# Kernel tuning notes

Hardware: AMD Instinct MI355X
Metric: run time of the kernel (lower is better)

The kernel has to match this reference:

```python
import jax, jax.numpy as jnp
import numpy as np

SEQ_LEN = 2048
N_FFT = 4096  # nearest power of two >= 2*SEQ_LEN - 1
K = 24
D_IN = 512
D_OUT = 512
K_U = 3


def setup_inputs() -> dict:
    key = jax.random.key(0)
    k1, k2, k3, k4, k5 = jax.random.split(key, 5)
    x = jax.random.normal(k1, (1, SEQ_LEN, D_IN), dtype=jnp.float32)
    phi = jax.random.normal(k2, (SEQ_LEN, K), dtype=jnp.float32)
    M = jax.random.normal(k3, (D_OUT, D_IN, K_U), dtype=jnp.float32) / D_IN
    M_phi_plus = jax.random.normal(k4, (K, D_IN, D_OUT), dtype=jnp.float32) / 10.0
    M_phi_minus = jax.random.normal(k5, (K, D_IN, D_OUT), dtype=jnp.float32) / 10.0
    return {"x": x, "phi": phi, "M": M, "M_phi_plus": M_phi_plus, "M_phi_minus": M_phi_minus}


def _convolve(u, v, n):
    # u: (bsz, seq, d_in); v: (seq, K) spectral filters
    bsz, seq_len, d_in = u.shape
    Kf = v.shape[1]
    # alternating sign (+1, -1, +1, ...) along time, shape (1, seq, 1, 1)
    sgn = jnp.where(jnp.arange(seq_len) % 2 == 1, -1.0, 1.0).reshape(1, seq_len, 1, 1)
    v_f = jnp.fft.rfft(v.astype(jnp.float32).reshape(1, seq_len, Kf, 1, 1), n=n, axis=1)
    u_exp = jnp.broadcast_to(u[:, :, None, :], (bsz, seq_len, Kf, d_in))
    # stack [u, u*sgn] -> (bsz, seq, K, d_in, 2)
    U = jnp.stack([u_exp, u_exp * sgn], axis=-1).astype(jnp.float32)
    U_f = jnp.fft.rfft(U, n=n, axis=1)
    U_conv = jnp.fft.irfft(v_f * U_f, n=n, axis=1)[:, :seq_len]
    U_plus = U_conv[..., 0]
    U_minus = U_conv[..., 1] * sgn  # (b, seq, K, d_in) * (1, seq, 1, 1)
    return U_plus, U_minus


def _ar_preds(M, x):
    # M: (d_out, d_in, k_u); x: (b, l, d_in)
    # ar[t] = sum_{i=0}^{k_u-1} M[:,:,i] @ x[t-i]  (zero before start)
    b, l, _ = x.shape
    out = jnp.zeros((b, l, M.shape[0]), dtype=x.dtype)
    for i in range(M.shape[-1]):
        x_shift = jnp.pad(x, ((0, 0), (i, 0), (0, 0)))[:, :l]
        out = out + jnp.einsum("bli,oi->blo", x_shift, M[:, :, i])
    return out


def reference(x, phi, M, M_phi_plus, M_phi_minus):
    U_plus, U_minus = _convolve(x, phi, N_FFT)
    spectral_plus = jnp.einsum("blkd,kdo->blo", U_plus, M_phi_plus)
    spectral_minus = jnp.einsum("blkd,kdo->blo", U_minus, M_phi_minus)
    output = spectral_plus + spectral_minus  # use_hankel_L=False
    ar = _ar_preds(M, x)
    return output + ar
```

## Files before the change

kernel.cpp:

```cpp
#include <hip/hip_runtime.h>

typedef __bf16 bf16;
typedef bf16 bf16x8 __attribute__((ext_vector_type(8)));
typedef float floatx16 __attribute__((ext_vector_type(16)));

#define AS1 __attribute__((address_space(1)))
#define AS3 __attribute__((address_space(3)))

#define KTOT 26112

__device__ __forceinline__ void stage_tile(const bf16* g, int ld, bf16* lds, int tid) {
#pragma unroll
    for (int it = 0; it < 4; ++it) {
        int q    = it * 256 + tid;
        int row  = q >> 3;
        int col8 = (q & 7) ^ (row & 7);
        __builtin_amdgcn_global_load_lds(
            (const AS1 void*)(g + (size_t)row * ld + col8 * 8),
            (AS3 void*)(lds + q * 8), 16, 0, 0);
    }
}

__device__ __forceinline__ void mfma_block(const bf16* lA, const bf16* lB,
                                           floatx16 acc[2][2], int lane, int wm, int wn) {
    const int lrow = lane & 31;
    const int lk   = lane >> 5;
#pragma unroll
    for (int s = 0; s < 4; ++s) {
        bf16x8 af[2], bfr[2];
        const int c8 = s * 2 + lk;
#pragma unroll
        for (int mi = 0; mi < 2; ++mi) {
            int r = wm * 64 + mi * 32 + lrow;
            af[mi] = *(const bf16x8*)(lA + r * 64 + ((c8 ^ (r & 7)) << 3));
        }
#pragma unroll
        for (int ni = 0; ni < 2; ++ni) {
            int r = wn * 64 + ni * 32 + lrow;
            bfr[ni] = *(const bf16x8*)(lB + r * 64 + ((c8 ^ (r & 7)) << 3));
        }
#pragma unroll
        for (int mi = 0; mi < 2; ++mi)
#pragma unroll
            for (int ni = 0; ni < 2; ++ni)
                acc[mi][ni] = __builtin_amdgcn_mfma_f32_32x32x16_bf16(
                    af[mi], bfr[ni], acc[mi][ni], 0, 0, 0);
    }
}

#define CD_ROW(r, lane) (((r) & 3) + 8 * ((r) >> 2) + 4 * ((lane) >> 5))

__global__ __launch_bounds__(256) void conv_gemm(const bf16* __restrict__ Tb,
                                                 const bf16* __restrict__ xT2,
                                                 bf16* __restrict__ A2) {
    __shared__ bf16 lA[128 * 64], lB[128 * 64];
    const int tid = threadIdx.x;
    const int lane = tid & 63, wave = tid >> 6, wm = wave & 1, wn = wave >> 1;
    const int bid = blockIdx.x;
    const int a    = 7 - (bid / 384);
    const int rem  = bid % 384;
    const int dblk = rem / 48;
    const int kw   = rem % 48;

    floatx16 acc[2][2];
#pragma unroll
    for (int mi = 0; mi < 2; ++mi)
#pragma unroll
        for (int ni = 0; ni < 2; ++ni)
#pragma unroll
            for (int e = 0; e < 16; ++e) acc[mi][ni][e] = 0.f;

    for (int c = 0; c <= a; ++c) {
        const bf16* Ab = Tb + ((size_t)kw * 8 + (a - c)) * 16384;
        const bf16* Bb = xT2 + (size_t)(dblk * 128) * 1024 + c * 128;
#pragma unroll
        for (int kk = 0; kk < 128; kk += 64) {
            stage_tile(Ab + kk, 128, lA, tid);
            stage_tile(Bb + kk, 1024, lB, tid);
            __syncthreads();
            mfma_block(lA, lB, acc, lane, wm, wn);
            __syncthreads();
        }
    }
    const int w = kw & 1, k = kw >> 1;
    const int kv = w ? (24 + k) : k;
    const int p = dblk >> 2, dbase = (dblk & 3) * 128;
    bf16* Ocol = A2 + (size_t)kv * 512 + dbase;
#pragma unroll
    for (int mi = 0; mi < 2; ++mi)
#pragma unroll
        for (int ni = 0; ni < 2; ++ni)
#pragma unroll
            for (int r = 0; r < 16; ++r) {
                int tau = a * 128 + wm * 64 + mi * 32 + CD_ROW(r, lane);
                int t = 2 * tau + p + w;
                if (t < 2048) {
                    int col = wn * 64 + ni * 32 + (lane & 31);
                    Ocol[(size_t)t * KTOT + col] = (bf16)acc[mi][ni][r];
                }
            }
}

__global__ __launch_bounds__(256) void proj_gemm(const bf16* __restrict__ A2,
                                                 const bf16* __restrict__ B2,
                                                 float* __restrict__ P2) {
    __shared__ bf16 lA[2][128 * 64], lB[2][128 * 64];
    const int tid = threadIdx.x;
    const int lane = tid & 63, wave = tid >> 6, wm = wave & 1, wn = wave >> 1;
    const int bm = blockIdx.x, sp = blockIdx.y, bn = blockIdx.z;
    const bf16* Ab = A2 + (size_t)bm * 128 * KTOT + sp * 3264;
    const bf16* Bb = B2 + (size_t)bn * 128 * KTOT + sp * 3264;

    floatx16 acc[2][2];
#pragma unroll
    for (int mi = 0; mi < 2; ++mi)
#pragma unroll
        for (int ni = 0; ni < 2; ++ni)
#pragma unroll
            for (int e = 0; e < 16; ++e) acc[mi][ni][e] = 0.f;

    stage_tile(Ab,      KTOT, lA[0], tid);
    stage_tile(Bb,      KTOT, lB[0], tid);
    stage_tile(Ab + 64, KTOT, lA[1], tid);
    stage_tile(Bb + 64, KTOT, lB[1], tid);

    int cur = 0;
    for (int t = 0; t < 50; ++t) {
        asm volatile("s_waitcnt vmcnt(8)" ::: "memory");
        __builtin_amdgcn_sched_barrier(0);
        __builtin_amdgcn_s_barrier();
        __builtin_amdgcn_sched_barrier(0);
        __builtin_amdgcn_s_setprio(1);
        mfma_block(lA[cur], lB[cur], acc, lane, wm, wn);
        __builtin_amdgcn_s_setprio(0);
        __builtin_amdgcn_sched_barrier(0);
        __builtin_amdgcn_s_barrier();
        __builtin_amdgcn_sched_barrier(0);
        if (t + 2 < 51) {
            stage_tile(Ab + (size_t)(t + 2) * 64, KTOT, lA[cur], tid);
            stage_tile(Bb + (size_t)(t + 2) * 64, KTOT, lB[cur], tid);
        }
        cur ^= 1;
    }
    asm volatile("s_waitcnt vmcnt(0)" ::: "memory");
    __builtin_amdgcn_sched_barrier(0);
    __builtin_amdgcn_s_barrier();
    __builtin_amdgcn_sched_barrier(0);
    mfma_block(lA[cur], lB[cur], acc, lane, wm, wn);

    float* Pt = P2 + (size_t)sp * 1048576;
#pragma unroll
    for (int mi = 0; mi < 2; ++mi)
#pragma unroll
        for (int ni = 0; ni < 2; ++ni)
#pragma unroll
            for (int r = 0; r < 16; ++r) {
                int t = bm * 128 + wm * 64 + mi * 32 + CD_ROW(r, lane);
                int o = bn * 128 + wn * 64 + ni * 32 + (lane & 31);
                Pt[(size_t)t * 512 + o] = acc[mi][ni][r];
            }
}

__global__ void prep_all(const float* __restrict__ x, const float* __restrict__ phi,
                         const float* __restrict__ M, const float* __restrict__ Mp,
                         const float* __restrict__ Mm, bf16* __restrict__ xT2,
                         bf16* __restrict__ A2, bf16* __restrict__ B2,
                         bf16* __restrict__ Tb) {
    __shared__ float smem[2][64 * 65];
    const int b = blockIdx.x, tid = threadIdx.x;
    if (b < 256) {
        int dpt = (b >> 4) * 64, st = (b & 15) * 64;
        int p = dpt >> 9, dbase = dpt & 511;
#pragma unroll
        for (int it = 0; it < 16; ++it) {
            int q = it * 256 + tid;
            int r = q >> 6, cc = q & 63;
            smem[0][r * 65 + cc] = x[(size_t)(2 * (st + r) + p) * 512 + dbase + cc];
        }
        __syncthreads();
#pragma unroll
        for (int it = 0; it < 2; ++it) {
            int q = it * 256 + tid;
            int r = q >> 3, c8 = q & 7;
            bf16x8 v;
#pragma unroll
            for (int jj = 0; jj < 8; ++jj)
                v[jj] = (bf16)smem[0][(c8 * 8 + jj) * 65 + r];
            *(bf16x8*)&xT2[(size_t)(dpt + r) * 1024 + st + c8 * 8] = v;
        }
    } else if (b < 1792) {
        int idx8 = (b - 256) * 256 + tid;
        int t = idx8 / 192, q = idx8 % 192;
        int i = q >> 6, d8 = (q & 63) * 8;
        bf16x8 v;
        if (t - i >= 0) {
            const float* xp = x + (size_t)(t - i) * 512 + d8;
            float4 f0 = *(const float4*)(xp);
            float4 f1 = *(const float4*)(xp + 4);
            v[0] = (bf16)f0.x; v[1] = (bf16)f0.y; v[2] = (bf16)f0.z; v[3] = (bf16)f0.w;
            v[4] = (bf16)f1.x; v[5] = (bf16)f1.y; v[6] = (bf16)f1.z; v[7] = (bf16)f1.w;
        } else {
#pragma unroll
            for (int jj = 0; jj < 8; ++jj) v[jj] = (bf16)0.f;
        }
        *(bf16x8*)(A2 + (size_t)t * KTOT + 24576 + i * 512 + d8) = v;
    } else if (b < 3328) {
        int b2 = b - 1792;
        int k = b2 >> 6, rem2 = b2 & 63;
        int dt = (rem2 >> 3) * 64, ot = (rem2 & 7) * 64;
        const float* Sp = Mp + (size_t)k * 262144;
        const float* Sm = Mm + (size_t)k * 262144;
#pragma unroll
        for (int it = 0; it < 16; ++it) {
            int q = it * 256 + tid;
            int r = q >> 6, cc = q & 63;
            smem[0][r * 65 + cc] = Sp[(size_t)(dt + r) * 512 + ot + cc];
            smem[1][r * 65 + cc] = Sm[(size_t)(dt + r) * 512 + ot + cc];
        }
        __syncthreads();
#pragma unroll
        for (int it = 0; it < 2; ++it) {
            int q = it * 256 + tid;
            int r = q >> 3, c8 = q & 7;
            bf16x8 vs, vd;
#pragma unroll
            for (int jj = 0; jj < 8; ++jj) {
                float av = smem[0][(c8 * 8 + jj) * 65 + r];
                float bv = smem[1][(c8 * 8 + jj) * 65 + r];
                vs[jj] = (bf16)(av + bv);
                vd[jj] = (bf16)(av - bv);
            }
            *(bf16x8*)&B2[(size_t)(ot + r) * KTOT + k * 512 + dt + c8 * 8] = vs;
            *(bf16x8*)&B2[(size_t)(ot + r) * KTOT + (24 + k) * 512 + dt + c8 * 8] = vd;
        }
    } else if (b < 3840) {
        int o = b - 3328;
        for (int q = tid; q < 1536; q += 256) smem[0][q] = M[(size_t)o * 1536 + q];
        __syncthreads();
        if (tid < 192) {
            int q = tid * 8;
            int i = q >> 9, d0 = q & 511;
            bf16x8 v;
#pragma unroll
            for (int jj = 0; jj < 8; ++jj) v[jj] = (bf16)smem[0][(d0 + jj) * 3 + i];
            *(bf16x8*)&B2[(size_t)o * KTOT + 24576 + q] = v;
        }
    } else if (b < 4224) {
        int b3 = b - 3840;
        int kw = b3 >> 3, m = b3 & 7;
        int k = kw >> 1, w = kw & 1;
        if (tid < 255) {
            int sh = m * 128 - 127 + tid;
            smem[0][tid] = (sh >= 0) ? phi[(size_t)(2 * sh + w) * 24 + k] : 0.f;
        }
        __syncthreads();
        bf16* Tp = Tb + (size_t)b3 * 16384;
#pragma unroll
        for (int it = 0; it < 8; ++it) {
            int q = it * 256 + tid;
            int i = q >> 4, j8 = (q & 15) * 8;
            bf16x8 v;
#pragma unroll
            for (int jj = 0; jj < 8; ++jj)
                v[jj] = (bf16)smem[0][127 + i - (j8 + jj)];
            *(bf16x8*)(Tp + i * 128 + j8) = v;
        }
    } else {
        int off = 12288 + (b - 4224) * 2048 + tid * 8;
        bf16x8 z;
#pragma unroll
        for (int jj = 0; jj < 8; ++jj) z[jj] = (bf16)0.f;
        *(bf16x8*)(A2 + off) = z;
    }
}

__global__ void reduce8(const float* __restrict__ P2, float* __restrict__ out) {
    int idx = blockIdx.x * 256 + threadIdx.x;
    if (idx >= 2048 * 512) return;
    float s = 0.f;
#pragma unroll
    for (int sp = 0; sp < 8; ++sp)
        s += P2[(size_t)sp * 1048576 + idx];
    out[idx] = s;
}

extern "C" void kernel_launch(void* const* d_in, const int* in_sizes, int n_in,
                              void* d_out, int out_size, void* d_ws, size_t ws_size,
                              hipStream_t stream) {
    const float* x   = (const float*)d_in[0];
    const float* phi = (const float*)d_in[1];
    const float* M   = (const float*)d_in[2];
    const float* Mp  = (const float*)d_in[3];
    const float* Mm  = (const float*)d_in[4];
    float* out = (float*)d_out;
    char* ws = (char*)d_ws;

    bf16*  Tb  = (bf16*)(ws + 0);
    bf16*  xT2 = (bf16*)(ws + 12582912);
    bf16*  A2  = (bf16*)(ws + 14680064);
    bf16*  B2  = (bf16*)(ws + 121634816);
    float* P2  = (float*)(ws + 148373504);

    prep_all<<<4230, 256, 0, stream>>>(x, phi, M, Mp, Mm, xT2, A2, B2, Tb);
    conv_gemm<<<3072, 256, 0, stream>>>(Tb, xT2, A2);
    proj_gemm<<<dim3(16, 8, 4), 256, 0, stream>>>(A2, B2, P2);
    reduce8<<<4096, 256, 0, stream>>>(P2, out);
}
```

Measured before the change: 256.0 us.

## Retile projection GEMM to 256x256 blocks with split-K atomics and triple buffering

Rewrites the projection GEMM to use 512-thread blocks with 256x256 output tiles, a K-step of 32 and a three-stage LDS ring. All LDS fragment reads are hoisted ahead of the MFMA sequence. The split-K dimension grows to 16 slices, and each slice accumulates directly into the output with float atomicAdd. This removes the partial-sum workspace and the separate reduce kernel, and prep_all now zeroes the output. The aim is more operand reuse per LDS load and no partial-buffer round trip, at the cost of many float atomics and a nondeterministic summation order.

```diff
diff --git a/kernel.cpp b/kernel.cpp
--- a/kernel.cpp
+++ b/kernel.cpp
@@ -101,63 +101,103 @@
             }
 }
 
-__global__ __launch_bounds__(256) void proj_gemm(const bf16* __restrict__ A2,
-                                                 const bf16* __restrict__ B2,
-                                                 float* __restrict__ P2) {
-    __shared__ bf16 lA[2][128 * 64], lB[2][128 * 64];
+__device__ __forceinline__ void stage32(const bf16* g, int ld, bf16* lds, int tid) {
+#pragma unroll
+    for (int it = 0; it < 2; ++it) {
+        int q    = it * 512 + tid;
+        int row  = q >> 2;
+        int col8 = (q & 3) ^ ((row >> 1) & 3);
+        __builtin_amdgcn_global_load_lds(
+            (const AS1 void*)(g + (size_t)row * ld + col8 * 8),
+            (AS3 void*)(lds + q * 8), 16, 0, 0);
+    }
+}
+
+__global__ __launch_bounds__(512, 2) void proj_gemm(const bf16* __restrict__ A2,
+                                                    const bf16* __restrict__ B2,
+                                                    float* __restrict__ out) {
+    __shared__ bf16 lA[3][256 * 32], lB[3][256 * 32];
     const int tid = threadIdx.x;
-    const int lane = tid & 63, wave = tid >> 6, wm = wave & 1, wn = wave >> 1;
-    const int bm = blockIdx.x, sp = blockIdx.y, bn = blockIdx.z;
-    const bf16* Ab = A2 + (size_t)bm * 128 * KTOT + sp * 3264;
-    const bf16* Bb = B2 + (size_t)bn * 128 * KTOT + sp * 3264;
-
-    floatx16 acc[2][2];
-#pragma unroll
-    for (int mi = 0; mi < 2; ++mi)
+    const int lane = tid & 63, w = tid >> 6;
+    const int wm = w >> 2, wn = w & 3;
+    const int lrow = lane & 31, lk = lane >> 5;
+    const int bm = blockIdx.x, bn = blockIdx.y, sp = blockIdx.z;
+    const bf16* Ab = A2 + (size_t)bm * 256 * KTOT + sp * 1632;
+    const bf16* Bb = B2 + (size_t)bn * 256 * KTOT + sp * 1632;
+
+    floatx16 acc[4][2];
+#pragma unroll
+    for (int mi = 0; mi < 4; ++mi)
 #pragma unroll
         for (int ni = 0; ni < 2; ++ni)
 #pragma unroll
             for (int e = 0; e < 16; ++e) acc[mi][ni][e] = 0.f;
 
-    stage_tile(Ab,      KTOT, lA[0], tid);
-    stage_tile(Bb,      KTOT, lB[0], tid);
-    stage_tile(Ab + 64, KTOT, lA[1], tid);
-    stage_tile(Bb + 64, KTOT, lB[1], tid);
-
-    int cur = 0;
-    for (int t = 0; t < 50; ++t) {
-        asm volatile("s_waitcnt vmcnt(8)" ::: "memory");
+    stage32(Ab,      KTOT, lA[0], tid);
+    stage32(Bb,      KTOT, lB[0], tid);
+    stage32(Ab + 32, KTOT, lA[1], tid);
+    stage32(Bb + 32, KTOT, lB[1], tid);
+
+    for (int t = 0; t < 51; ++t) {
+        const int b = t % 3;
+        if (t + 2 < 51) {
+            stage32(Ab + (size_t)(t + 2) * 32, KTOT, lA[(t + 2) % 3], tid);
+            stage32(Bb + (size_t)(t + 2) * 32, KTOT, lB[(t + 2) % 3], tid);
+        }
+        if (t < 49) {
+            asm volatile("s_waitcnt vmcnt(8)" ::: "memory");
+        } else if (t == 49) {
+            asm volatile("s_waitcnt vmcnt(4)" ::: "memory");
+        } else {
+            asm volatile("s_waitcnt vmcnt(0)" ::: "memory");
+        }
         __builtin_amdgcn_sched_barrier(0);
         __builtin_amdgcn_s_barrier();
         __builtin_amdgcn_sched_barrier(0);
+
+        const bf16* LA = lA[b];
+        const bf16* LB = lB[b];
+        bf16x8 af[4][2], bfr[2][2];
+#pragma unroll
+        for (int s = 0; s < 2; ++s) {
+            const int c8 = s * 2 + lk;
+#pragma unroll
+            for (int mi = 0; mi < 4; ++mi) {
+                int r = wm * 128 + mi * 32 + lrow;
+                af[mi][s] = *(const bf16x8*)(LA + r * 32 + ((c8 ^ ((r >> 1) & 3)) << 3));
+            }
+#pragma unroll
+            for (int ni = 0; ni < 2; ++ni) {
+                int r = wn * 64 + ni * 32 + lrow;
+                bfr[ni][s] = *(const bf16x8*)(LB + r * 32 + ((c8 ^ ((r >> 1) & 3)) << 3));
+            }
+        }
+        asm volatile("s_waitcnt lgkmcnt(0)" ::: "memory");
+        __builtin_amdgcn_sched_barrier(0);
         __builtin_amdgcn_s_setprio(1);
-        mfma_block(lA[cur], lB[cur], acc, lane, wm, wn);
+#pragma unroll
+        for (int s = 0; s < 2; ++s)
+#pragma unroll
+            for (int mi = 0; mi < 4; ++mi)
+#pragma unroll
+                for (int ni = 0; ni < 2; ++ni)
+                    acc[mi][ni] = __builtin_amdgcn_mfma_f32_32x32x16_bf16(
+                        af[mi][s], bfr[ni][s], acc[mi][ni], 0, 0, 0);
         __builtin_amdgcn_s_setprio(0);
         __builtin_amdgcn_sched_barrier(0);
         __builtin_amdgcn_s_barrier();
         __builtin_amdgcn_sched_barrier(0);
-        if (t + 2 < 51) {
-            stage_tile(Ab + (size_t)(t + 2) * 64, KTOT, lA[cur], tid);
-            stage_tile(Bb + (size_t)(t + 2) * 64, KTOT, lB[cur], tid);
-        }
-        cur ^= 1;
-    }
-    asm volatile("s_waitcnt vmcnt(0)" ::: "memory");
-    __builtin_amdgcn_sched_barrier(0);
-    __builtin_amdgcn_s_barrier();
-    __builtin_amdgcn_sched_barrier(0);
-    mfma_block(lA[cur], lB[cur], acc, lane, wm, wn);
-
-    float* Pt = P2 + (size_t)sp * 1048576;
-#pragma unroll
-    for (int mi = 0; mi < 2; ++mi)
+    }
+
+#pragma unroll
+    for (int mi = 0; mi < 4; ++mi)
 #pragma unroll
         for (int ni = 0; ni < 2; ++ni)
 #pragma unroll
             for (int r = 0; r < 16; ++r) {
-                int t = bm * 128 + wm * 64 + mi * 32 + CD_ROW(r, lane);
-                int o = bn * 128 + wn * 64 + ni * 32 + (lane & 31);
-                Pt[(size_t)t * 512 + o] = acc[mi][ni][r];
+                int trow = bm * 256 + wm * 128 + mi * 32 + CD_ROW(r, lane);
+                int o    = bn * 256 + wn * 64 + ni * 32 + (lane & 31);
+                atomicAdd(out + (size_t)trow * 512 + o, acc[mi][ni][r]);
             }
 }
 
@@ -165,7 +205,7 @@
                          const float* __restrict__ M, const float* __restrict__ Mp,
                          const float* __restrict__ Mm, bf16* __restrict__ xT2,
                          bf16* __restrict__ A2, bf16* __restrict__ B2,
-                         bf16* __restrict__ Tb) {
+                         bf16* __restrict__ Tb, float* __restrict__ out) {
     __shared__ float smem[2][64 * 65];
     const int b = blockIdx.x, tid = threadIdx.x;
     if (b < 256) {
@@ -265,23 +305,18 @@
                 v[jj] = (bf16)smem[0][127 + i - (j8 + jj)];
             *(bf16x8*)(Tp + i * 128 + j8) = v;
         }
-    } else {
+    } else if (b < 4230) {
         int off = 12288 + (b - 4224) * 2048 + tid * 8;
         bf16x8 z;
 #pragma unroll
         for (int jj = 0; jj < 8; ++jj) z[jj] = (bf16)0.f;
         *(bf16x8*)(A2 + off) = z;
-    }
-}
-
-__global__ void reduce8(const float* __restrict__ P2, float* __restrict__ out) {
-    int idx = blockIdx.x * 256 + threadIdx.x;
-    if (idx >= 2048 * 512) return;
-    float s = 0.f;
-#pragma unroll
-    for (int sp = 0; sp < 8; ++sp)
-        s += P2[(size_t)sp * 1048576 + idx];
-    out[idx] = s;
+    } else {
+        int idx = ((b - 4230) * 256 + tid) * 8;
+        float4 z4 = make_float4(0.f, 0.f, 0.f, 0.f);
+        *(float4*)(out + idx)     = z4;
+        *(float4*)(out + idx + 4) = z4;
+    }
 }
 
 extern "C" void kernel_launch(void* const* d_in, const int* in_sizes, int n_in,
@@ -299,10 +334,8 @@
     bf16*  xT2 = (bf16*)(ws + 12582912);
     bf16*  A2  = (bf16*)(ws + 14680064);
     bf16*  B2  = (bf16*)(ws + 121634816);
-    float* P2  = (float*)(ws + 148373504);
-
-    prep_all<<<4230, 256, 0, stream>>>(x, phi, M, Mp, Mm, xT2, A2, B2, Tb);
+
+    prep_all<<<4742, 256, 0, stream>>>(x, phi, M, Mp, Mm, xT2, A2, B2, Tb, out);
     conv_gemm<<<3072, 256, 0, stream>>>(Tb, xT2, A2);
-    proj_gemm<<<dim3(16, 8, 4), 256, 0, stream>>>(A2, B2, P2);
-    reduce8<<<4096, 256, 0, stream>>>(P2, out);
-}
+    proj_gemm<<<dim3(8, 2, 16), 512, 0, stream>>>(A2, B2, out);
+}
```

Result: slower. 280.9 us (+9.7%).
